# Kernel tuning notes

Measured on AMD Instinct MI355X. Metric: run time of the kernel, lower is better.

The kernel has to match this reference:

```python
import jax, jax.numpy as jnp
import numpy as np

NODES = 16384                       # power of two -> all heap levels complete
DEPTH = (NODES - 1).bit_length() + 1  # 15 heap steps, linears k = 0..14
IN_F = 64
OUT_F = 64
MINHEAP = 0
BATCH = 32


def setup_inputs() -> dict:
    key = jax.random.key(0)
    k1, k2, k3 = jax.random.split(key, 3)
    x = jax.random.normal(k1, (BATCH, NODES, IN_F), dtype=jnp.float32)
    # stacked per-heap-step Linear params, torch layout W: [out, in]
    W = jax.random.normal(k2, (DEPTH - MINHEAP, OUT_F, IN_F), dtype=jnp.float32) * 0.05
    b = jax.random.normal(k3, (DEPTH - MINHEAP, OUT_F), dtype=jnp.float32) * 0.05
    return {"x": x, "W": W, "b": b}


def reference(x, W, b):
    # HeapLinear forward. Heap layout: level l occupies nodes [2^(l-1), 2^l)
    # (root = node 0, level(j) = bit_length(j)). The original double loop over
    # (input level l, linear k) with repeat_interleave(2^k) is equivalent to:
    #   output[j] = sum_{k=minheap}^{depth-1, level(j)>=k} linears[k](input[j >> k])
    # for power-of-two `nodes` (every out block satisfies out_node1 <= nodes).
    nodes = x.shape[-2]
    depth = (nodes - 1).bit_length() + 1
    j = np.arange(nodes)
    levels = np.array([int(v).bit_length() for v in j])  # static, trace-time
    out = jnp.zeros(x.shape[:-1] + (W.shape[1],), dtype=x.dtype)
    for k in range(MINHEAP, depth):
        n_anc = max(nodes >> k, 1)  # only nodes 0..n_anc-1 serve as distance-k ancestors
        # small per-level Linear applied to ancestor slice: [..., n_anc, out]
        t = jnp.einsum('...ni,oi->...no', x[..., :n_anc, :], W[k - MINHEAP]) + b[k - MINHEAP]
        anc = j >> k                      # distance-k ancestor of each node
        mask = levels >= k                # nodes shallower than k have no such ancestor
        out = out + jnp.where(mask[:, None], t[..., anc, :], jnp.zeros((), x.dtype))
    return out
```

## Files before the change

kernel.cpp:

```cpp
#include <hip/hip_runtime.h>

#define NODES 16384
#define NF 64
#define NBLK 128
#define TROW 72
#define BATCH 32

#define WS_XSWZ_OFF   0ull
#define WS_WBF_OFF    67108864ull
#define WS_BPRE_OFF   67231744ull
#define WS_NEEDED     67235584ull

typedef __attribute__((ext_vector_type(8))) short short8;
typedef __attribute__((ext_vector_type(4))) short shortx4;
typedef __attribute__((ext_vector_type(4))) float floatx4;

__device__ __forceinline__ short f2bf(float f) {
    unsigned u = __float_as_uint(f);
    u += 0x7fffu + ((u >> 16) & 1u);
    return (short)(u >> 16);
}
__device__ __forceinline__ float bf2f(short s) {
    return __uint_as_float(((unsigned)(unsigned short)s) << 16);
}
__device__ __forceinline__ short8 cvt8(floatx4 a, floatx4 c) {
    short8 r;
    r[0]=f2bf(a[0]); r[1]=f2bf(a[1]); r[2]=f2bf(a[2]); r[3]=f2bf(a[3]);
    r[4]=f2bf(c[0]); r[5]=f2bf(c[1]); r[6]=f2bf(c[2]); r[7]=f2bf(c[3]);
    return r;
}

__global__ __launch_bounds__(256)
void heaplin_prep(const float* __restrict__ x, const float* __restrict__ W,
                  const float* __restrict__ bias,
                  short* __restrict__ xswz, short* __restrict__ wbf,
                  float* __restrict__ bpre)
{
    const int blk = blockIdx.x;
    const int tid = threadIdx.x;
    if (blk < 16384) {
        int g  = blk * 256 + tid;
        int p  = g & 127;
        int tg = g >> 7;
        const float* src = x + ((size_t)(tg << 4) + (p & 15)) * NF + (p >> 4) * 8;
        floatx4 a = *(const floatx4*)src;
        floatx4 c = *(const floatx4*)(src + 4);
        *(short8*)(xswz + (size_t)g * 8) = cvt8(a, c);
    } else if (blk < 16414) {
        int e = (blk - 16384) * 2048 + tid * 8;
        floatx4 a = *(const floatx4*)(W + e);
        floatx4 c = *(const floatx4*)(W + e + 4);
        *(short8*)(wbf + e) = cvt8(a, c);
    } else {
        if (tid < 64) {
            float run = 0.f;
            for (int k = 0; k < 15; ++k) { run += bias[k * 64 + tid]; bpre[k * 64 + tid] = run; }
        }
    }
}

__global__ __launch_bounds__(256, 4)
void heaplin_main(const float* __restrict__ x, const float* __restrict__ W,
                  const short* __restrict__ xswz, const short* __restrict__ wbf,
                  const float* __restrict__ bpre, float* __restrict__ out)
{
    __shared__ short tbuf[128 * TROW];
    __shared__ float farpart[4 * 64];

    const int tid  = threadIdx.x;
    const int lane = tid & 63;
    const int wave = tid >> 6;
    const int lr = lane & 15;
    const int lq = lane >> 4;
    const int nblk = blockIdx.x;
    const int b    = blockIdx.y;
    const float* xb = x + (size_t)b * NODES * NF;
    const short* xsb = xswz + (size_t)b * NODES * NF;
    float* ob = out + (size_t)b * NODES * NF;
    const floatx4 zero4 = {0.f, 0.f, 0.f, 0.f};

    if (nblk == 0) {
        floatx4 accE[8];
        #pragma unroll
        for (int t8 = 0; t8 < 8; ++t8) accE[t8] = zero4;

        for (int k = 0; k < 8; ++k) {
            __syncthreads();
            #pragma unroll
            for (int i = 0; i < 8; ++i) {
                int job = tid + i * 256;
                int r = job >> 4, c4 = job & 15;
                bool valid = (k == 0) || (r >= (1 << (k - 1)));
                floatx4 vv = zero4;
                if (valid) vv = *(const floatx4*)(xb + (r >> k) * NF + c4 * 4);
                shortx4 s4;
                s4[0]=f2bf(vv[0]); s4[1]=f2bf(vv[1]); s4[2]=f2bf(vv[2]); s4[3]=f2bf(vv[3]);
                *(shortx4*)(tbuf + r * TROW + c4 * 4) = s4;
            }
            __syncthreads();
            #pragma unroll
            for (int t8 = 0; t8 < 8; ++t8) {
                int mt = 2 * wave + (t8 & 1);
                int nt = t8 >> 1;
                int arow = mt * 16 + lr;
                const short* wp = wbf + k * 4096 + (nt * 16 + lr) * 64 + lq * 8;
                short8 b0 = *(const short8*)wp;
                short8 b1 = *(const short8*)(wp + 32);
                short8 a0 = *(const short8*)(tbuf + arow * TROW + lq * 8);
                short8 a1 = *(const short8*)(tbuf + arow * TROW + 32 + lq * 8);
                accE[t8] = __builtin_amdgcn_mfma_f32_16x16x32_bf16(a0, b0, accE[t8], 0, 0, 0);
                accE[t8] = __builtin_amdgcn_mfma_f32_16x16x32_bf16(a1, b1, accE[t8], 0, 0, 0);
            }
        }
        #pragma unroll
        for (int t8 = 0; t8 < 8; ++t8) {
            int mt = 2 * wave + (t8 & 1);
            int nt = t8 >> 1;
            int c = nt * 16 + lr;
            #pragma unroll
            for (int rg = 0; rg < 4; ++rg) {
                int j = mt * 16 + lq * 4 + rg;
                int lvl = (j == 0) ? 0 : (32 - __clz(j));
                ob[(size_t)j * NF + c] = accE[t8][rg] + bpre[lvl * 64 + c];
            }
        }
        return;
    }

    const int n0 = nblk * NBLK;
    const int L  = 32 - __clz(n0);

    floatx4 accE[8];
    const short* xtile0 = xsb + (size_t)(n0 >> 4) * 1024;
    #pragma unroll
    for (int t8 = 0; t8 < 8; ++t8) {
        int mt = 2 * wave + (t8 & 1);
        int nt = t8 >> 1;
        const short* ap = xtile0 + mt * 1024 + lane * 8;
        short8 a0 = *(const short8*)ap;
        short8 a1 = *(const short8*)(ap + 512);
        const short* wp = wbf + (nt * 16 + lr) * 64 + lq * 8;
        short8 b0 = *(const short8*)wp;
        short8 b1 = *(const short8*)(wp + 32);
        floatx4 acc = zero4;
        acc = __builtin_amdgcn_mfma_f32_16x16x32_bf16(a0, b0, acc, 0, 0, 0);
        acc = __builtin_amdgcn_mfma_f32_16x16x32_bf16(a1, b1, acc, 0, 0, 0);
        accE[t8] = acc;
    }

    {
        float p = 0.f;
        const int q = wave, o = lane;
        for (int k = 8; k <= L; ++k) {
            const float* xa = xb + (size_t)(n0 >> k) * NF + q * 16;
            const float* wr = W + k * 4096 + o * 64 + q * 16;
            #pragma unroll
            for (int i = 0; i < 4; ++i) {
                floatx4 wv = *(const floatx4*)(wr + i * 4);
                floatx4 xv = *(const floatx4*)(xa + i * 4);
                p += wv[0]*xv[0] + wv[1]*xv[1] + wv[2]*xv[2] + wv[3]*xv[3];
            }
        }
        if (q == 0) p += bpre[L * 64 + o];
        farpart[q * 64 + o] = p;
    }

    for (int jj = 0; jj < 11; ++jj) {
        int job = wave * 11 + jj;
        int idx = job >> 2;
        int nt  = job & 3;
        int k, mt;
        if (idx < 4)       { k = 1; mt = idx; }
        else if (idx < 6)  { k = 2; mt = idx - 4; }
        else if (idx == 6) { k = 3; mt = 0; }
        else               { k = idx - 3; mt = 0; }
        int anc = n0 >> k;
        int T   = (anc >> 4) + mt;
        int off = anc & 15;
        const short* ap = xsb + (size_t)T * 1024 + lane * 8;
        short8 a0 = *(const short8*)ap;
        short8 a1 = *(const short8*)(ap + 512);
        const short* wp = wbf + k * 4096 + (nt * 16 + lr) * 64 + lq * 8;
        short8 b0 = *(const short8*)wp;
        short8 b1 = *(const short8*)(wp + 32);
        floatx4 acc = zero4;
        acc = __builtin_amdgcn_mfma_f32_16x16x32_bf16(a0, b0, acc, 0, 0, 0);
        acc = __builtin_amdgcn_mfma_f32_16x16x32_bf16(a1, b1, acc, 0, 0, 0);
        int tb  = 128 - (256 >> k);
        int cnt = 128 >> k;
        #pragma unroll
        for (int rg = 0; rg < 4; ++rg) {
            int m = lq * 4 + rg;
            if (k <= 3) {
                tbuf[(tb + mt * 16 + m) * TROW + nt * 16 + lr] = f2bf(acc[rg]);
            } else if (m >= off && m < off + cnt) {
                tbuf[(tb + m - off) * TROW + nt * 16 + lr] = f2bf(acc[rg]);
            }
        }
    }
    __syncthreads();

    {
        int m  = tid >> 2;
        int c0 = (tid & 3) * 16;
        float e[16];
        #pragma unroll
        for (int i = 0; i < 16; ++i) {
            int c = c0 + i;
            e[i] = bf2f(tbuf[ m               * TROW + c])
                 + bf2f(tbuf[(64  + (m >> 1)) * TROW + c])
                 + bf2f(tbuf[(96  + (m >> 2)) * TROW + c])
                 + bf2f(tbuf[(112 + (m >> 3)) * TROW + c])
                 + bf2f(tbuf[(120 + (m >> 4)) * TROW + c])
                 + bf2f(tbuf[(124 + (m >> 5)) * TROW + c])
                 + bf2f(tbuf[126              * TROW + c])
                 + farpart[c] + farpart[64 + c] + farpart[128 + c] + farpart[192 + c];
        }
        #pragma unroll
        for (int i = 0; i < 16; ++i) tbuf[m * TROW + c0 + i] = f2bf(e[i]);
    }
    __syncthreads();

    #pragma unroll
    for (int t8 = 0; t8 < 8; ++t8) {
        int mt = 2 * wave + (t8 & 1);
        int nt = t8 >> 1;
        int c = nt * 16 + lr;
        #pragma unroll
        for (int rg = 0; rg < 4; ++rg) {
            int j = mt * 16 + lq * 4 + rg;
            float val = accE[t8][rg] + bf2f(tbuf[(j >> 1) * TROW + c]);
            ob[(size_t)(n0 + j) * NF + c] = val;
        }
    }
}

#define SROW 72
#define SROWS 270
__global__ __launch_bounds__(256, 4)
void heaplin_fallback(const float* __restrict__ x, const float* __restrict__ W,
                      const float* __restrict__ bias, float* __restrict__ out)
{
    __shared__ short stage[SROWS * SROW];
    __shared__ float farpart[4 * 64];
    short* tbuf = stage;
    float* cumB = (float*)(stage + 128 * SROW);

    const int tid  = threadIdx.x;
    const int lane = tid & 63;
    const int wave = tid >> 6;
    const int lr = lane & 15;
    const int lq = lane >> 4;
    const int nblk = blockIdx.x;
    const int b    = blockIdx.y;
    const float* xb = x + (size_t)b * NODES * NF;
    float* ob = out + (size_t)b * NODES * NF;
    const floatx4 zero4 = {0.f, 0.f, 0.f, 0.f};

    if (nblk == 0) {
        if (tid < 64) {
            float run = 0.f;
            for (int k = 0; k < 15; ++k) { run += bias[k * 64 + tid]; cumB[k * 64 + tid] = run; }
        }
        floatx4 accE[8];
        #pragma unroll
        for (int t8 = 0; t8 < 8; ++t8) accE[t8] = zero4;
        for (int k = 0; k < 8; ++k) {
            __syncthreads();
            #pragma unroll
            for (int i = 0; i < 8; ++i) {
                int job = tid + i * 256;
                int r = job >> 4, c4 = job & 15;
                bool valid = (k == 0) || (r >= (1 << (k - 1)));
                floatx4 vv = zero4;
                if (valid) vv = *(const floatx4*)(xb + (r >> k) * NF + c4 * 4);
                shortx4 s4;
                s4[0]=f2bf(vv[0]); s4[1]=f2bf(vv[1]); s4[2]=f2bf(vv[2]); s4[3]=f2bf(vv[3]);
                *(shortx4*)(stage + r * SROW + c4 * 4) = s4;
            }
            __syncthreads();
            #pragma unroll
            for (int t8 = 0; t8 < 8; ++t8) {
                int mt = 2 * wave + (t8 & 1);
                int nt = t8 >> 1;
                int arow = mt * 16 + lr;
                const float* wr = W + k * 4096 + (nt * 16 + lr) * 64 + lq * 8;
                floatx4 wa = *(const floatx4*)wr, wb2 = *(const floatx4*)(wr + 4);
                short8 b0 = cvt8(wa, wb2);
                floatx4 wc = *(const floatx4*)(wr + 32), wd = *(const floatx4*)(wr + 36);
                short8 b1 = cvt8(wc, wd);
                short8 a0 = *(const short8*)(stage + arow * SROW + lq * 8);
                short8 a1 = *(const short8*)(stage + arow * SROW + 32 + lq * 8);
                accE[t8] = __builtin_amdgcn_mfma_f32_16x16x32_bf16(a0, b0, accE[t8], 0, 0, 0);
                accE[t8] = __builtin_amdgcn_mfma_f32_16x16x32_bf16(a1, b1, accE[t8], 0, 0, 0);
            }
        }
        #pragma unroll
        for (int t8 = 0; t8 < 8; ++t8) {
            int mt = 2 * wave + (t8 & 1);
            int nt = t8 >> 1;
            int c = nt * 16 + lr;
            #pragma unroll
            for (int rg = 0; rg < 4; ++rg) {
                int j = mt * 16 + lq * 4 + rg;
                int lvl = (j == 0) ? 0 : (32 - __clz(j));
                ob[(size_t)j * NF + c] = accE[t8][rg] + cumB[lvl * 64 + c];
            }
        }
        return;
    }

    const int n0 = nblk * NBLK;
    const int L  = 32 - __clz(n0);
    floatx4 v[16];
    #pragma unroll
    for (int i = 0; i < 16; ++i) {
        int job = tid + i * 256;
        int r = job >> 4, c4 = job & 15;
        int node;
        if (r < 128)        node = n0 + r;
        else if (r >= 254)  node = n0 >> 7;
        else { int k = __clz(255 - r) - 24; node = (n0 >> k) + r - (256 - (256 >> k)); }
        v[i] = *(const floatx4*)(xb + (size_t)node * NF + c4 * 4);
    }
    #pragma unroll
    for (int i = 0; i < 16; ++i) {
        int job = tid + i * 256;
        int r = job >> 4, c4 = job & 15;
        shortx4 s4;
        s4[0]=f2bf(v[i][0]); s4[1]=f2bf(v[i][1]); s4[2]=f2bf(v[i][2]); s4[3]=f2bf(v[i][3]);
        *(shortx4*)(stage + r * SROW + c4 * 4) = s4;
    }
    __syncthreads();
    floatx4 accE[8];
    #pragma unroll
    for (int t8 = 0; t8 < 8; ++t8) {
        int mt = 2 * wave + (t8 & 1);
        int nt = t8 >> 1;
        int arow = mt * 16 + lr;
        const float* wr = W + (nt * 16 + lr) * 64 + lq * 8;
        floatx4 wa = *(const floatx4*)wr, wb2 = *(const floatx4*)(wr + 4);
        short8 b0 = cvt8(wa, wb2);
        floatx4 wc = *(const floatx4*)(wr + 32), wd = *(const floatx4*)(wr + 36);
        short8 b1 = cvt8(wc, wd);
        short8 a0 = *(const short8*)(stage + arow * SROW + lq * 8);
        short8 a1 = *(const short8*)(stage + arow * SROW + 32 + lq * 8);
        floatx4 acc = zero4;
        acc = __builtin_amdgcn_mfma_f32_16x16x32_bf16(a0, b0, acc, 0, 0, 0);
        acc = __builtin_amdgcn_mfma_f32_16x16x32_bf16(a1, b1, acc, 0, 0, 0);
        accE[t8] = acc;
    }
    {
        float p = 0.f;
        const int q = wave, o = lane;
        for (int k = 8; k <= L; ++k) {
            const float* xa = xb + (size_t)(n0 >> k) * NF + q * 16;
            const float* wr = W + k * 4096 + o * 64 + q * 16;
            #pragma unroll
            for (int i = 0; i < 4; ++i) {
                floatx4 wv = *(const floatx4*)(wr + i * 4);
                floatx4 xv = *(const floatx4*)(xa + i * 4);
                p += wv[0]*xv[0] + wv[1]*xv[1] + wv[2]*xv[2] + wv[3]*xv[3];
            }
        }
        if (q == 0) for (int k = 0; k <= L; ++k) p += bias[k * 64 + o];
        farpart[q * 64 + o] = p;
    }
    __syncthreads();
    for (int jj = 0; jj < 11; ++jj) {
        int job = wave + jj * 4;
        int idx = job % 11;
        int nt  = job / 11;
        int k, mt;
        if (idx < 4)      { k = 1; mt = idx; }
        else if (idx < 6) { k = 2; mt = idx - 4; }
        else if (idx < 7) { k = 3; mt = 0; }
        else              { k = idx - 3; mt = 0; }
        int sbase = 256 - (256 >> k);
        int arow = sbase + mt * 16 + lr;
        const float* wr = W + k * 4096 + (nt * 16 + lr) * 64 + lq * 8;
        floatx4 wa = *(const floatx4*)wr, wb2 = *(const floatx4*)(wr + 4);
        short8 b0 = cvt8(wa, wb2);
        floatx4 wc = *(const floatx4*)(wr + 32), wd = *(const floatx4*)(wr + 36);
        short8 b1 = cvt8(wc, wd);
        short8 a0 = *(const short8*)(stage + arow * SROW + lq * 8);
        short8 a1 = *(const short8*)(stage + arow * SROW + 32 + lq * 8);
        floatx4 acc = zero4;
        acc = __builtin_amdgcn_mfma_f32_16x16x32_bf16(a0, b0, acc, 0, 0, 0);
        acc = __builtin_amdgcn_mfma_f32_16x16x32_bf16(a1, b1, acc, 0, 0, 0);
        int tb = 128 - (256 >> k);
        int nvalid = 128 >> k;
        #pragma unroll
        for (int rg = 0; rg < 4; ++rg) {
            int m = mt * 16 + lq * 4 + rg;
            if (m < nvalid) tbuf[(tb + m) * TROW + nt * 16 + lr] = f2bf(acc[rg]);
        }
    }
    __syncthreads();
    {
        int m  = tid >> 2;
        int c0 = (tid & 3) * 16;
        float e[16];
        #pragma unroll
        for (int i = 0; i < 16; ++i) {
            int c = c0 + i;
            e[i] = bf2f(tbuf[ m               * TROW + c])
                 + bf2f(tbuf[(64  + (m >> 1)) * TROW + c])
                 + bf2f(tbuf[(96  + (m >> 2)) * TROW + c])
                 + bf2f(tbuf[(112 + (m >> 3)) * TROW + c])
                 + bf2f(tbuf[(120 + (m >> 4)) * TROW + c])
                 + bf2f(tbuf[(124 + (m >> 5)) * TROW + c])
                 + bf2f(tbuf[126              * TROW + c])
                 + farpart[c] + farpart[64 + c] + farpart[128 + c] + farpart[192 + c];
        }
        #pragma unroll
        for (int i = 0; i < 16; ++i) tbuf[m * TROW + c0 + i] = f2bf(e[i]);
    }
    __syncthreads();
    #pragma unroll
    for (int t8 = 0; t8 < 8; ++t8) {
        int mt = 2 * wave + (t8 & 1);
        int nt = t8 >> 1;
        int c = nt * 16 + lr;
        #pragma unroll
        for (int rg = 0; rg < 4; ++rg) {
            int j = mt * 16 + lq * 4 + rg;
            float val = accE[t8][rg] + bf2f(tbuf[(j >> 1) * TROW + c]);
            ob[(size_t)(n0 + j) * NF + c] = val;
        }
    }
}

extern "C" void kernel_launch(void* const* d_in, const int* in_sizes, int n_in,
                              void* d_out, int out_size, void* d_ws, size_t ws_size,
                              hipStream_t stream) {
    const float* x  = (const float*)d_in[0];
    const float* W  = (const float*)d_in[1];
    const float* bs = (const float*)d_in[2];
    float* out = (float*)d_out;
    dim3 grid(NODES / NBLK, BATCH);
    if (ws_size >= WS_NEEDED) {
        short* xswz = (short*)((char*)d_ws + WS_XSWZ_OFF);
        short* wbf  = (short*)((char*)d_ws + WS_WBF_OFF);
        float* bpre = (float*)((char*)d_ws + WS_BPRE_OFF);
        heaplin_prep<<<16415, 256, 0, stream>>>(x, W, bs, xswz, wbf, bpre);
        heaplin_main<<<grid, 256, 0, stream>>>(x, W, xswz, wbf, bpre, out);
    } else {
        heaplin_fallback<<<grid, 256, 0, stream>>>(x, W, bs, out);
    }
}
```

Baseline: 358.4 us.

## Drop bf16 pre-swizzle of x; convert fp32 x in-register inside main kernel

Removes the prep pass that wrote a full bf16-swizzled copy of x to workspace, so the main kernel now loads fp32 x directly and converts it to bf16 in registers before the MFMAs. This drops a full read and write of x plus the later reread of the bf16 copy, at the cost of reading fp32 (twice the bytes) in the main kernel. The ancestor MFMA jobs are regrouped so each wave loads an A tile once and reuses it across four column tiles. The far-ancestor loop is unrolled to a fixed count with predication, and launch bounds drop to 2 blocks per SM to allow more registers.

Result: no change. 353.5 us (-1.4%).

```diff
diff --git a/kernel.cpp b/kernel.cpp
--- a/kernel.cpp
+++ b/kernel.cpp
@@ -6,10 +6,9 @@
 #define TROW 72
 #define BATCH 32
 
-#define WS_XSWZ_OFF   0ull
-#define WS_WBF_OFF    67108864ull
-#define WS_BPRE_OFF   67231744ull
-#define WS_NEEDED     67235584ull
+#define WS_WBF_OFF    0ull
+#define WS_BPRE_OFF   122880ull
+#define WS_NEEDED     126720ull
 
 typedef __attribute__((ext_vector_type(8))) short short8;
 typedef __attribute__((ext_vector_type(4))) short shortx4;
@@ -31,37 +30,25 @@
 }
 
 __global__ __launch_bounds__(256)
-void heaplin_prep(const float* __restrict__ x, const float* __restrict__ W,
-                  const float* __restrict__ bias,
-                  short* __restrict__ xswz, short* __restrict__ wbf,
-                  float* __restrict__ bpre)
+void heaplin_prep(const float* __restrict__ W, const float* __restrict__ bias,
+                  short* __restrict__ wbf, float* __restrict__ bpre)
 {
     const int blk = blockIdx.x;
     const int tid = threadIdx.x;
-    if (blk < 16384) {
-        int g  = blk * 256 + tid;
-        int p  = g & 127;
-        int tg = g >> 7;
-        const float* src = x + ((size_t)(tg << 4) + (p & 15)) * NF + (p >> 4) * 8;
-        floatx4 a = *(const floatx4*)src;
-        floatx4 c = *(const floatx4*)(src + 4);
-        *(short8*)(xswz + (size_t)g * 8) = cvt8(a, c);
-    } else if (blk < 16414) {
-        int e = (blk - 16384) * 2048 + tid * 8;
+    if (blk < 30) {
+        int e = blk * 2048 + tid * 8;
         floatx4 a = *(const floatx4*)(W + e);
         floatx4 c = *(const floatx4*)(W + e + 4);
         *(short8*)(wbf + e) = cvt8(a, c);
-    } else {
-        if (tid < 64) {
-            float run = 0.f;
-            for (int k = 0; k < 15; ++k) { run += bias[k * 64 + tid]; bpre[k * 64 + tid] = run; }
-        }
-    }
-}
-
-__global__ __launch_bounds__(256, 4)
+    } else if (tid < 64) {
+        float run = 0.f;
+        for (int k = 0; k < 15; ++k) { run += bias[k * 64 + tid]; bpre[k * 64 + tid] = run; }
+    }
+}
+
+__global__ __launch_bounds__(256, 2)
 void heaplin_main(const float* __restrict__ x, const float* __restrict__ W,
-                  const short* __restrict__ xswz, const short* __restrict__ wbf,
+                  const short* __restrict__ wbf,
                   const float* __restrict__ bpre, float* __restrict__ out)
 {
     __shared__ short tbuf[128 * TROW];
@@ -75,7 +62,6 @@
     const int nblk = blockIdx.x;
     const int b    = blockIdx.y;
     const float* xb = x + (size_t)b * NODES * NF;
-    const short* xsb = xswz + (size_t)b * NODES * NF;
     float* ob = out + (size_t)b * NODES * NF;
     const floatx4 zero4 = {0.f, 0.f, 0.f, 0.f};
 
@@ -131,70 +117,87 @@
     const int L  = 32 - __clz(n0);
 
     floatx4 accE[8];
-    const short* xtile0 = xsb + (size_t)(n0 >> 4) * 1024;
-    #pragma unroll
-    for (int t8 = 0; t8 < 8; ++t8) {
-        int mt = 2 * wave + (t8 & 1);
-        int nt = t8 >> 1;
-        const short* ap = xtile0 + mt * 1024 + lane * 8;
-        short8 a0 = *(const short8*)ap;
-        short8 a1 = *(const short8*)(ap + 512);
-        const short* wp = wbf + (nt * 16 + lr) * 64 + lq * 8;
-        short8 b0 = *(const short8*)wp;
-        short8 b1 = *(const short8*)(wp + 32);
-        floatx4 acc = zero4;
-        acc = __builtin_amdgcn_mfma_f32_16x16x32_bf16(a0, b0, acc, 0, 0, 0);
-        acc = __builtin_amdgcn_mfma_f32_16x16x32_bf16(a1, b1, acc, 0, 0, 0);
-        accE[t8] = acc;
+    {
+        const float* apA = xb + (size_t)(n0 + 2 * wave * 16 + lr) * NF + lq * 8;
+        const float* apB = apA + 16 * NF;
+        floatx4 fA0 = *(const floatx4*)apA,        fA1 = *(const floatx4*)(apA + 4);
+        floatx4 fA2 = *(const floatx4*)(apA + 32), fA3 = *(const floatx4*)(apA + 36);
+        floatx4 fB0 = *(const floatx4*)apB,        fB1 = *(const floatx4*)(apB + 4);
+        floatx4 fB2 = *(const floatx4*)(apB + 32), fB3 = *(const floatx4*)(apB + 36);
+        short8 aA0 = cvt8(fA0, fA1), aA1 = cvt8(fA2, fA3);
+        short8 aB0 = cvt8(fB0, fB1), aB1 = cvt8(fB2, fB3);
+        #pragma unroll
+        for (int nt = 0; nt < 4; ++nt) {
+            const short* wp = wbf + (nt * 16 + lr) * 64 + lq * 8;
+            short8 b0 = *(const short8*)wp;
+            short8 b1 = *(const short8*)(wp + 32);
+            floatx4 accA = zero4, accB = zero4;
+            accA = __builtin_amdgcn_mfma_f32_16x16x32_bf16(aA0, b0, accA, 0, 0, 0);
+            accA = __builtin_amdgcn_mfma_f32_16x16x32_bf16(aA1, b1, accA, 0, 0, 0);
+            accB = __builtin_amdgcn_mfma_f32_16x16x32_bf16(aB0, b0, accB, 0, 0, 0);
+            accB = __builtin_amdgcn_mfma_f32_16x16x32_bf16(aB1, b1, accB, 0, 0, 0);
+            accE[2 * nt + 0] = accA;
+            accE[2 * nt + 1] = accB;
+        }
     }
 
     {
         float p = 0.f;
         const int q = wave, o = lane;
-        for (int k = 8; k <= L; ++k) {
+        #pragma unroll
+        for (int k = 8; k <= 14; ++k) {
             const float* xa = xb + (size_t)(n0 >> k) * NF + q * 16;
             const float* wr = W + k * 4096 + o * 64 + q * 16;
+            float s = 0.f;
             #pragma unroll
             for (int i = 0; i < 4; ++i) {
                 floatx4 wv = *(const floatx4*)(wr + i * 4);
                 floatx4 xv = *(const floatx4*)(xa + i * 4);
-                p += wv[0]*xv[0] + wv[1]*xv[1] + wv[2]*xv[2] + wv[3]*xv[3];
-            }
+                s += wv[0]*xv[0] + wv[1]*xv[1] + wv[2]*xv[2] + wv[3]*xv[3];
+            }
+            p += (k <= L) ? s : 0.f;
         }
         if (q == 0) p += bpre[L * 64 + o];
         farpart[q * 64 + o] = p;
     }
 
-    for (int jj = 0; jj < 11; ++jj) {
-        int job = wave * 11 + jj;
-        int idx = job >> 2;
-        int nt  = job & 3;
+    #pragma unroll
+    for (int g = 0; g < 3; ++g) {
+        const int idx = wave + g * 4;
+        const bool gvalid = (idx < 11);
+        const int idxc = gvalid ? idx : 0;
         int k, mt;
-        if (idx < 4)       { k = 1; mt = idx; }
-        else if (idx < 6)  { k = 2; mt = idx - 4; }
-        else if (idx == 6) { k = 3; mt = 0; }
-        else               { k = idx - 3; mt = 0; }
-        int anc = n0 >> k;
-        int T   = (anc >> 4) + mt;
-        int off = anc & 15;
-        const short* ap = xsb + (size_t)T * 1024 + lane * 8;
-        short8 a0 = *(const short8*)ap;
-        short8 a1 = *(const short8*)(ap + 512);
-        const short* wp = wbf + k * 4096 + (nt * 16 + lr) * 64 + lq * 8;
-        short8 b0 = *(const short8*)wp;
-        short8 b1 = *(const short8*)(wp + 32);
-        floatx4 acc = zero4;
-        acc = __builtin_amdgcn_mfma_f32_16x16x32_bf16(a0, b0, acc, 0, 0, 0);
-        acc = __builtin_amdgcn_mfma_f32_16x16x32_bf16(a1, b1, acc, 0, 0, 0);
-        int tb  = 128 - (256 >> k);
-        int cnt = 128 >> k;
-        #pragma unroll
-        for (int rg = 0; rg < 4; ++rg) {
-            int m = lq * 4 + rg;
-            if (k <= 3) {
-                tbuf[(tb + mt * 16 + m) * TROW + nt * 16 + lr] = f2bf(acc[rg]);
-            } else if (m >= off && m < off + cnt) {
-                tbuf[(tb + m - off) * TROW + nt * 16 + lr] = f2bf(acc[rg]);
+        if (idxc < 4)       { k = 1; mt = idxc; }
+        else if (idxc < 6)  { k = 2; mt = idxc - 4; }
+        else if (idxc == 6) { k = 3; mt = 0; }
+        else                { k = idxc - 3; mt = 0; }
+        const int anc = n0 >> k;
+        const int rowb = (anc & ~15) + mt * 16;
+        const float* ap = xb + (size_t)(rowb + lr) * NF + lq * 8;
+        floatx4 f0 = *(const floatx4*)ap,        f1 = *(const floatx4*)(ap + 4);
+        floatx4 f2 = *(const floatx4*)(ap + 32), f3 = *(const floatx4*)(ap + 36);
+        short8 a0 = cvt8(f0, f1), a1 = cvt8(f2, f3);
+        const int tb  = 128 - (256 >> k);
+        const int cnt = 128 >> k;
+        const int off = anc & 15;
+        #pragma unroll
+        for (int nt = 0; nt < 4; ++nt) {
+            const short* wp = wbf + k * 4096 + (nt * 16 + lr) * 64 + lq * 8;
+            short8 b0 = *(const short8*)wp;
+            short8 b1 = *(const short8*)(wp + 32);
+            floatx4 acc = zero4;
+            acc = __builtin_amdgcn_mfma_f32_16x16x32_bf16(a0, b0, acc, 0, 0, 0);
+            acc = __builtin_amdgcn_mfma_f32_16x16x32_bf16(a1, b1, acc, 0, 0, 0);
+            if (gvalid) {
+                #pragma unroll
+                for (int rg = 0; rg < 4; ++rg) {
+                    int m = lq * 4 + rg;
+                    if (k <= 3) {
+                        tbuf[(tb + mt * 16 + m) * TROW + nt * 16 + lr] = f2bf(acc[rg]);
+                    } else if (m >= off && m < off + cnt) {
+                        tbuf[(tb + m - off) * TROW + nt * 16 + lr] = f2bf(acc[rg]);
+                    }
+                }
             }
         }
     }
@@ -440,11 +443,10 @@
     float* out = (float*)d_out;
     dim3 grid(NODES / NBLK, BATCH);
     if (ws_size >= WS_NEEDED) {
-        short* xswz = (short*)((char*)d_ws + WS_XSWZ_OFF);
         short* wbf  = (short*)((char*)d_ws + WS_WBF_OFF);
         float* bpre = (float*)((char*)d_ws + WS_BPRE_OFF);
-        heaplin_prep<<<16415, 256, 0, stream>>>(x, W, bs, xswz, wbf, bpre);
-        heaplin_main<<<grid, 256, 0, stream>>>(x, W, xswz, wbf, bpre, out);
+        heaplin_prep<<<31, 256, 0, stream>>>(W, bs, wbf, bpre);
+        heaplin_main<<<grid, 256, 0, stream>>>(x, W, wbf, bpre, out);
     } else {
         heaplin_fallback<<<grid, 256, 0, stream>>>(x, W, bs, out);
     }
```
